# Kernel tuning notes

Hardware: AMD Instinct MI355X
Metric: run time of the kernel (lower is better)

## Reference

```python
import jax, jax.numpy as jnp
import numpy as np

B, T, F, H = 2048, 16, 768, 1024  # batch(nodes), timesteps, 3*input_size, hidden_size


def setup_inputs() -> dict:
    key = jax.random.key(0)
    k1, k2, k3 = jax.random.split(key, 3)
    s_ih = 1.0 / np.sqrt(F)
    s_hh = 1.0 / np.sqrt(H)
    return {
        "x": jax.random.normal(k1, (B, T, F), dtype=jnp.float32),
        "W_ih": jax.random.normal(k2, (F, 4 * H), dtype=jnp.float32) * s_ih,
        "W_hh": jax.random.normal(k3, (H, 4 * H), dtype=jnp.float32) * s_hh,
        "b": jnp.zeros((4 * H,), dtype=jnp.float32),
    }


def reference(x, W_ih, W_hh, b):
    # Batched equivalent of the original per-sample python loop:
    # each sample's [T, F] sequence runs through the LSTM; the final hidden
    # state [H] per sample is concatenated and reshaped to (-1, B).
    Bb, Tt, Ff = x.shape
    Hh = W_hh.shape[0]
    x_t = jnp.swapaxes(x, 0, 1)  # [T, B, F]

    def step(carry, xt):
        h, c = carry
        gates = xt @ W_ih + h @ W_hh + b  # [B, 4H]
        i, f, g, o = jnp.split(gates, 4, axis=-1)
        c = jax.nn.sigmoid(f) * c + jax.nn.sigmoid(i) * jnp.tanh(g)
        h = jax.nn.sigmoid(o) * jnp.tanh(c)
        return (h, c), None

    h0 = jnp.zeros((Bb, Hh), dtype=x.dtype)
    (h, _), _ = jax.lax.scan(step, (h0, h0), x_t)
    # torch.cat over batch of [H] vectors -> flat [B*H], then reshape(-1, B)
    return h.reshape(-1).reshape(-1, Bb)
```

## Files before the change

kernel.cpp:

```cpp
#include <hip/hip_runtime.h>
#include <hip/hip_bf16.h>
#include <stdint.h>

#define B_  2048
#define T_  16
#define F_  768
#define H_  1024
#define G4_ 4096

typedef __attribute__((ext_vector_type(8))) __bf16 bf16x8;
typedef __attribute__((ext_vector_type(4))) float  f32x4;

static __device__ __forceinline__ unsigned short f2bf(float f) {
    union { float f; uint32_t u; } v; v.f = f;
    uint32_t u = v.u;
    uint32_t r = (u + 0x7fffu + ((u >> 16) & 1u)) >> 16;
    return (unsigned short)r;
}
static __device__ __forceinline__ unsigned short f2h(float f) {
    union { _Float16 h; unsigned short u; } v; v.h = (_Float16)f; return v.u;
}
static __device__ __forceinline__ float h2f(unsigned short u) {
    union { _Float16 h; unsigned short u; } v; v.u = u; return (float)v.h;
}
static __device__ __forceinline__ float sigf(float x) {
    return 1.0f / (1.0f + __expf(-x));
}
static __device__ __forceinline__ float tanhfast(float x) {
    return 2.0f / (1.0f + __expf(-2.0f * x)) - 1.0f;
}

#define GLOAD_LDS16(gsrc, ldst)                                                       \
    __builtin_amdgcn_global_load_lds((const __attribute__((address_space(1))) void*)(gsrc), \
                                     (__attribute__((address_space(3))) void*)(ldst), \
                                     16, 0, 0)


__global__ void convert_x_kernel(const float* __restrict__ x,
                                 unsigned short* __restrict__ xbf, int n4) {
    int idx = blockIdx.x * blockDim.x + threadIdx.x;
    if (idx >= n4) return;
    float4 v = *(const float4*)(x + (size_t)idx * 4);
    ushort4 o;
    o.x = f2bf(v.x); o.y = f2bf(v.y); o.z = f2bf(v.z); o.w = f2bf(v.w);
    *(ushort4*)(xbf + (size_t)idx * 4) = o;
}

__global__ void transpose_w_kernel(const float* __restrict__ w,
                                   unsigned short* __restrict__ wt, int K, int mode) {
    __shared__ float tile[32][33];
    int nb = blockIdx.x * 32;
    int kb = blockIdx.y * 32;
    int tx = threadIdx.x, ty = threadIdx.y;
    #pragma unroll
    for (int i = 0; i < 32; i += 8)
        tile[ty + i][tx] = w[(size_t)(kb + ty + i) * G4_ + nb + tx];
    __syncthreads();
    #pragma unroll
    for (int i = 0; i < 32; i += 8) {
        int n = nb + ty + i;
        int g = n >> 10;
        int j = n & 1023;
        int np = mode ? ((j >> 4) * 64 + g * 16 + (j & 15))
                      : ((j >> 6) * 256 + g * 64 + ((j >> 4) & 3) * 16 + (j & 15));
        wt[(size_t)np * K + kb + tx] = f2bf(tile[tx][ty + i]);
    }
}


#define STAGE4(bufi, kind, half, gbase, ld, rowbase, kt) do {                         \
    const int kel_ = (kt) * 64;                                                       \
    _Pragma("unroll")                                                                 \
    for (int r2 = 0; r2 < 2; ++r2) {                                                  \
        const int rih_ = r2 * 64 + (tid >> 3);                                        \
        const int ch_  = (tid & 7) ^ (rih_ & 7);                                      \
        GLOAD_LDS16((gbase) + (size_t)((rowbase) + (half) * 128 + rih_) * (ld)        \
                            + kel_ + ch_ * 8,                                         \
                    &lds[bufi][kind][half][r2 * 4096 + tid * 8]);                     \
    }                                                                                 \
} while (0)

#define RD4_A(half_, mb)                                                              \
    _Pragma("unroll")                                                                 \
    for (int mm = 0; mm < 4; ++mm) {                                                  \
        const int row_ = ((mb) + mm) * 32 + wm * 16 + fr;                             \
        _Pragma("unroll")                                                             \
        for (int kk = 0; kk < 2; ++kk)                                                \
            Afr[mm][kk] = *(const bf16x8*)&lds[buf][0][half_]                         \
                [(row_ & 127) * 64 + (((kk * 4 + fq) ^ (row_ & 7)) * 8)];             \
    }

#define RD4_B(half_, nb)                                                              \
    _Pragma("unroll")                                                                 \
    for (int nn = 0; nn < 2; ++nn) {                                                  \
        const int row_ = ((nb) + nn) * 64 + wn * 16 + fr;                             \
        _Pragma("unroll")                                                             \
        for (int kk = 0; kk < 2; ++kk)                                                \
            Bfr[(nb) + nn][kk] = *(const bf16x8*)&lds[buf][1][half_]                  \
                [(row_ & 127) * 64 + (((kk * 4 + fq) ^ (row_ & 7)) * 8)];             \
    }

#define MFMAQ(mb, nb)                                                                 \
    __builtin_amdgcn_s_setprio(1);                                                    \
    _Pragma("unroll")                                                                 \
    for (int mm = 0; mm < 4; ++mm)                                                    \
        _Pragma("unroll")                                                             \
        for (int nn = 0; nn < 2; ++nn)                                                \
            _Pragma("unroll")                                                         \
            for (int kk = 0; kk < 2; ++kk)                                            \
                acc[(mb) + mm][(nb) + nn] = __builtin_amdgcn_mfma_f32_16x16x32_bf16(  \
                    Afr[mm][kk], Bfr[(nb) + nn][kk], acc[(mb) + mm][(nb) + nn], 0, 0, 0); \
    __builtin_amdgcn_s_setprio(0);

#define WAITV4  asm volatile("s_waitcnt vmcnt(10)" ::: "memory");                     \
                __builtin_amdgcn_sched_barrier(0);
#define BARR4   __builtin_amdgcn_s_barrier();                                         \
                __builtin_amdgcn_sched_barrier(0);

#define EPIX(pbn)                                                                     \
    {                                                                                 \
        const int j_ = (pbn) * 64 + wn * 16 + fr;                                     \
        _Pragma("unroll")                                                             \
        for (int mm = 0; mm < 8; ++mm) {                                              \
            _Pragma("unroll")                                                         \
            for (int rr = 0; rr < 4; ++rr) {                                          \
                int row_ = bm0 + mm * 32 + wm * 16 + fq * 4 + rr;                     \
                int tt_ = row_ & 15, bb_ = row_ >> 4;                                 \
                ushort4 o_;                                                           \
                o_.x = f2h(acc[mm][0][rr]);                                           \
                o_.y = f2h(acc[mm][1][rr]);                                           \
                o_.z = f2h(acc[mm][2][rr]);                                           \
                o_.w = f2h(acc[mm][3][rr]);                                           \
                *(ushort4*)(gx + (((size_t)tt_ * B_ + bb_) * H_ + j_) * 4) = o_;      \
            }                                                                         \
        }                                                                             \
    }

__global__ __launch_bounds__(512, 2) void xgemm8p_kernel(
        const unsigned short* __restrict__ xbf,
        const unsigned short* __restrict__ wih_t,
        unsigned short* __restrict__ gx) {
    __shared__ __align__(16) unsigned short lds[2][2][2][8192];

    const int bid = blockIdx.x;
    const int xcd = bid & 7;
    const int i   = bid >> 3;
    const int bnp = i & 7;
    const int bm  = xcd * 16 + (i >> 3);
    const int bm0 = bm * 256;
    const int bn00 = bnp * 512;

    const int tid = threadIdx.x;
    const int wid = tid >> 6, lane = tid & 63;
    const int wm = wid >> 2, wn = wid & 3;
    const int fr = lane & 15, fq = lane >> 4;

    f32x4 acc[8][4] = {};

    STAGE4(0, 0, 0, xbf, F_, bm0, 0);
    STAGE4(0, 1, 0, wih_t, F_, bn00, 0);
    STAGE4(0, 1, 1, wih_t, F_, bn00, 0);
    STAGE4(0, 0, 1, xbf, F_, bm0, 0);
    STAGE4(1, 0, 0, xbf, F_, bm0, 1);
    STAGE4(1, 1, 0, wih_t, F_, bn00, 1);
    STAGE4(1, 1, 1, wih_t, F_, bn00, 1);
    WAITV4; BARR4;

    for (int kt = 0; kt < 24; ++kt) {
        const int buf = kt & 1, nbuf = buf ^ 1;
        const int k1 = (kt + 1 < 24) ? kt + 1 : 23;
        const int k2 = (kt + 2 < 24) ? kt + 2 : 23;
        const int a1 = (k1 >= 12) ? k1 - 12 : k1;
        const int a2 = (k2 >= 12) ? k2 - 12 : k2;
        const int bb2 = bn00 + ((k2 >= 12) ? 256 : 0);
        bf16x8 Afr[4][2]; bf16x8 Bfr[4][2];
        RD4_A(0, 0); RD4_B(0, 0);
        STAGE4(nbuf, 0, 1, xbf, F_, bm0, a1);
        WAITV4; BARR4;
        MFMAQ(0, 0); BARR4;
        RD4_B(1, 2);
        STAGE4(buf, 0, 0, xbf, F_, bm0, a2);
        WAITV4; BARR4;
        MFMAQ(0, 2); BARR4;
        RD4_A(1, 4);
        STAGE4(buf, 1, 0, wih_t, F_, bb2, a2);
        BARR4;
        MFMAQ(4, 0); BARR4;
        STAGE4(buf, 1, 1, wih_t, F_, bb2, a2);
        WAITV4; BARR4;
        MFMAQ(4, 2); BARR4;
        if (kt == 11) {
            EPIX(bnp * 2);
            #pragma unroll
            for (int mm = 0; mm < 8; ++mm)
                #pragma unroll
                for (int nf = 0; nf < 4; ++nf)
                    #pragma unroll
                    for (int q = 0; q < 4; ++q) acc[mm][nf][q] = 0.0f;
        }
    }
    EPIX(bnp * 2 + 1);
}


#define STA6(slot, kt) do {                                                           \
    const int kel_ = (kt) * 64;                                                       \
    _Pragma("unroll")                                                                 \
    for (int r2 = 0; r2 < 2; ++r2) {                                                  \
        const int rih_ = r2 * 32 + (tid >> 3);                                        \
        const int ch_  = (tid & 7) ^ (rih_ & 7);                                      \
        GLOAD_LDS16(hprev + (size_t)(bm0 + rih_) * H_ + kel_ + ch_ * 8,               \
                    &ldsA[slot][r2 * 2048 + tid * 8]);                                \
    }                                                                                 \
} while (0)

#define STB6(slot, rowbase, kt) do {                                                  \
    const int kel_ = (kt) * 64;                                                       \
    _Pragma("unroll")                                                                 \
    for (int r4 = 0; r4 < 4; ++r4) {                                                  \
        const int rih_ = r4 * 32 + (tid >> 3);                                        \
        const int ch_  = (tid & 7) ^ (rih_ & 7);                                      \
        GLOAD_LDS16(whh_t + (size_t)((rowbase) + rih_) * H_ + kel_ + ch_ * 8,         \
                    &ldsB[slot][r4 * 2048 + tid * 8]);                                \
    }                                                                                 \
} while (0)

#define RD_A6(slot, AR)                                                               \
    _Pragma("unroll")                                                                 \
    for (int mm = 0; mm < 2; ++mm) {                                                  \
        const int row_ = wm * 32 + mm * 16 + fr;                                      \
        _Pragma("unroll")                                                             \
        for (int kk = 0; kk < 2; ++kk)                                                \
            AR[mm][kk] = *(const bf16x8*)&ldsA[slot]                                  \
                [row_ * 64 + (((kk * 4 + fq) ^ (row_ & 7)) * 8)];                     \
    }

#define RD_B6(slot, BF)                                                               \
    _Pragma("unroll")                                                                 \
    for (int nf = 0; nf < 4; ++nf) {                                                  \
        const int rowb_ = wn * 64 + nf * 16 + fr;                                     \
        _Pragma("unroll")                                                             \
        for (int kk = 0; kk < 2; ++kk)                                                \
            BF[nf][kk] = *(const bf16x8*)&ldsB[slot]                                  \
                [rowb_ * 64 + (((kk * 4 + fq) ^ (rowb_ & 7)) * 8)];                   \
    }

#define MFMA16S(AR, BF)                                                               \
    __builtin_amdgcn_s_setprio(1);                                                    \
    _Pragma("unroll")                                                                 \
    for (int mm = 0; mm < 2; ++mm)                                                    \
        _Pragma("unroll")                                                             \
        for (int nf = 0; nf < 4; ++nf)                                                \
            _Pragma("unroll")                                                         \
            for (int kk = 0; kk < 2; ++kk)                                            \
                acc[mm][nf] = __builtin_amdgcn_mfma_f32_16x16x32_bf16(                \
                    AR[mm][kk], BF[nf][kk], acc[mm][nf], 0, 0, 0);                    \
    __builtin_amdgcn_s_setprio(0);

#define LGKM0 asm volatile("s_waitcnt lgkmcnt(0)" ::: "memory");
#define BARR  __builtin_amdgcn_s_barrier();

__global__ __launch_bounds__(256, 2) void lstm_step_dp_kernel(
        const unsigned short* __restrict__ hprev,
        const unsigned short* __restrict__ whh_t,
        const unsigned short* __restrict__ gx,
        const float* __restrict__ bias,
        float* __restrict__ c,
        unsigned short* __restrict__ hnext,
        float* __restrict__ hout,
        int t, int last) {
    __shared__ __align__(16) unsigned short ldsA[3][4096];
    __shared__ __align__(16) unsigned short ldsB[3][8192];

    const int bid = blockIdx.x;
    const int xcd = bid & 7;
    const int i   = bid >> 3;
    const int pair = i & 1;
    const int bm  = i >> 1;
    const int bn_base = xcd * 4 + pair * 2;
    const int bm0 = bm * 64;

    const int tid = threadIdx.x;
    const int wid = tid >> 6, lane = tid & 63;
    const int wm = wid >> 1, wn = wid & 1;
    const int fr = lane & 15, fq = lane >> 4;

    const int j0 = (bn_base * 2 + wn) * 16 + fr;
    const int j1 = ((bn_base + 1) * 2 + wn) * 16 + fr;
    const float bi0 = bias[j0], bf0 = bias[H_ + j0], bg0 = bias[2 * H_ + j0], bo0 = bias[3 * H_ + j0];
    const float bi1 = bias[j1], bf1 = bias[H_ + j1], bg1 = bias[2 * H_ + j1], bo1 = bias[3 * H_ + j1];

    f32x4 acc[2][4] = {};
    ushort4 gpre[2][4];
    float   cpre[2][4];

    STA6(0, 0); STB6(0, bn_base * 128, 0);
    STA6(1, 1); STB6(1, bn_base * 128, 1);
    asm volatile("s_waitcnt vmcnt(6)" ::: "memory");
    BARR;

    for (int kt = 0; kt < 32; ++kt) {
        const int s_  = kt % 3;
        const int s2_ = (kt + 2) % 3;
        const int k2  = (kt + 2 < 32) ? kt + 2 : 31;
        const int ak2 = k2 & 15;
        const int brb2 = (bn_base + (k2 >> 4)) * 128;
        bf16x8 Am[2][2], Bf[4][2];
        RD_A6(s_, Am);
        RD_B6(s_, Bf);
        STA6(s2_, ak2);
        STB6(s2_, brb2, ak2);
        if (kt == 13 || kt == 29) {
            const int p_ = kt >> 4;
            const int jp_ = p_ ? j1 : j0;
            #pragma unroll
            for (int mm = 0; mm < 2; ++mm)
                #pragma unroll
                for (int rr = 0; rr < 4; ++rr) {
                    int row_ = bm0 + wm * 32 + mm * 16 + fq * 4 + rr;
                    gpre[mm][rr] = *(const ushort4*)(gx + (((size_t)t * B_ + row_) * H_ + jp_) * 4);
                    cpre[mm][rr] = c[(size_t)row_ * H_ + jp_];
                }
        }
        LGKM0;
        MFMA16S(Am, Bf);
        if (kt == 13 || kt == 14 || kt == 29 || kt == 30)
            asm volatile("s_waitcnt vmcnt(22)" ::: "memory");
        else
            asm volatile("s_waitcnt vmcnt(6)" ::: "memory");
        BARR;
        if (kt == 15) {
            #pragma unroll
            for (int mm = 0; mm < 2; ++mm) {
                #pragma unroll
                for (int rr = 0; rr < 4; ++rr) {
                    int row_ = bm0 + wm * 32 + mm * 16 + fq * 4 + rr;
                    ushort4 g4 = gpre[mm][rr];
                    float gi = acc[mm][0][rr] + bi0 + h2f(g4.x);
                    float gf = acc[mm][1][rr] + bf0 + h2f(g4.y);
                    float gg = acc[mm][2][rr] + bg0 + h2f(g4.z);
                    float go = acc[mm][3][rr] + bo0 + h2f(g4.w);
                    float cn = sigf(gf) * cpre[mm][rr] + sigf(gi) * tanhfast(gg);
                    float hv = sigf(go) * tanhfast(cn);
                    size_t off = (size_t)row_ * H_ + j0;
                    c[off] = cn;
                    hnext[off] = f2bf(hv);
                    if (last) hout[off] = hv;
                }
            }
            #pragma unroll
            for (int mm = 0; mm < 2; ++mm)
                #pragma unroll
                for (int nf = 0; nf < 4; ++nf)
                    #pragma unroll
                    for (int q = 0; q < 4; ++q) acc[mm][nf][q] = 0.0f;
        }
    }

    #pragma unroll
    for (int mm = 0; mm < 2; ++mm) {
        #pragma unroll
        for (int rr = 0; rr < 4; ++rr) {
            int row_ = bm0 + wm * 32 + mm * 16 + fq * 4 + rr;
            ushort4 g4 = gpre[mm][rr];
            float gi = acc[mm][0][rr] + bi1 + h2f(g4.x);
            float gf = acc[mm][1][rr] + bf1 + h2f(g4.y);
            float gg = acc[mm][2][rr] + bg1 + h2f(g4.z);
            float go = acc[mm][3][rr] + bo1 + h2f(g4.w);
            float cn = sigf(gf) * cpre[mm][rr] + sigf(gi) * tanhfast(gg);
            float hv = sigf(go) * tanhfast(cn);
            size_t off = (size_t)row_ * H_ + j1;
            c[off] = cn;
            hnext[off] = f2bf(hv);
            if (last) hout[off] = hv;
        }
    }
}


__global__ void cell0_kernel(const unsigned short* __restrict__ gx,
                             const float* __restrict__ bias,
                             float* __restrict__ c,
                             unsigned short* __restrict__ hbf) {
    int idx = blockIdx.x * blockDim.x + threadIdx.x;
    int b = idx >> 10;
    int j = idx & 1023;
    ushort4 g4 = *(const ushort4*)(gx + ((size_t)b * H_ + j) * 4);
    float gi = bias[j]          + h2f(g4.x);
    float gg = bias[2 * H_ + j] + h2f(g4.z);
    float go = bias[3 * H_ + j] + h2f(g4.w);
    float cn = sigf(gi) * tanhfast(gg);
    float hv = sigf(go) * tanhfast(cn);
    size_t off = (size_t)b * H_ + j;
    c[off] = cn;
    hbf[off] = f2bf(hv);
}


extern "C" void kernel_launch(void* const* d_in, const int* in_sizes, int n_in,
                              void* d_out, int out_size, void* d_ws, size_t ws_size,
                              hipStream_t stream) {
    const float* x    = (const float*)d_in[0];
    const float* Wih  = (const float*)d_in[1];
    const float* Whh  = (const float*)d_in[2];
    const float* bias = (const float*)d_in[3];
    float* out = (float*)d_out;

    char* ws = (char*)d_ws;
    unsigned short* xbf   = (unsigned short*)(ws);
    unsigned short* wih_t = (unsigned short*)(ws + 50331648);
    unsigned short* whh_t = (unsigned short*)(ws + 56623104);
    unsigned short* hbf0  = (unsigned short*)(ws + 65011712);
    unsigned short* hbf1  = (unsigned short*)(ws + 69206016);
    float*          c     = (float*)(ws + 73400320);
    unsigned short* gx    = (unsigned short*)(ws + 81788928);

    int n4 = B_ * T_ * F_ / 4;
    hipLaunchKernelGGL(convert_x_kernel, dim3((n4 + 255) / 256), dim3(256), 0, stream,
                       x, xbf, n4);
    hipLaunchKernelGGL(transpose_w_kernel, dim3(G4_ / 32, F_ / 32), dim3(32, 8), 0, stream,
                       Wih, wih_t, F_, 0);
    hipLaunchKernelGGL(transpose_w_kernel, dim3(G4_ / 32, H_ / 32), dim3(32, 8), 0, stream,
                       Whh, whh_t, H_, 1);

    hipLaunchKernelGGL(xgemm8p_kernel, dim3(1024), dim3(512), 0, stream,
                       xbf, wih_t, gx);

    hipLaunchKernelGGL(cell0_kernel, dim3(B_ * H_ / 256), dim3(256), 0, stream,
                       gx, bias, c, hbf0);

    for (int t = 1; t < T_; ++t) {
        unsigned short* hr = (t & 1) ? hbf0 : hbf1;
        unsigned short* hw = (t & 1) ? hbf1 : hbf0;
        hipLaunchKernelGGL(lstm_step_dp_kernel, dim3(512), dim3(256), 0, stream,
                           hr, whh_t, gx, bias, c, hw, out, t, (t == T_ - 1) ? 1 : 0);
    }
}
```

Measured before the change: 841.1 us.

## Fuse prep kernels into one launch and fold cell0 into the input GEMM

Merges the x conversion and the two weight transposes into a single block-indexed prep kernel. Restructures the input-projection GEMM so each block computes a single 256-column tile over 2048 blocks, replacing the earlier scheme of two tiles per block with a mid-loop epilogue. Fuses the t=0 LSTM cell update into the GEMM epilogue, so timestep-0 gates are never written to or re-read from global memory and the separate cell0 launch disappears. The cost removed is launch overhead and one gx round trip; the risk is a different tile schedule and occupancy for the GEMM.

Result: faster. 736.9 us (-12.4%).

```diff
diff --git a/kernel.cpp b/kernel.cpp
--- a/kernel.cpp
+++ b/kernel.cpp
@@ -36,22 +36,28 @@
                                      16, 0, 0)
 
 
-__global__ void convert_x_kernel(const float* __restrict__ x,
-                                 unsigned short* __restrict__ xbf, int n4) {
-    int idx = blockIdx.x * blockDim.x + threadIdx.x;
-    if (idx >= n4) return;
-    float4 v = *(const float4*)(x + (size_t)idx * 4);
-    ushort4 o;
-    o.x = f2bf(v.x); o.y = f2bf(v.y); o.z = f2bf(v.z); o.w = f2bf(v.w);
-    *(ushort4*)(xbf + (size_t)idx * 4) = o;
-}
-
-__global__ void transpose_w_kernel(const float* __restrict__ w,
-                                   unsigned short* __restrict__ wt, int K, int mode) {
+__global__ void prep_kernel(const float* __restrict__ x, unsigned short* __restrict__ xbf,
+                            const float* __restrict__ Wih, unsigned short* __restrict__ wih_t,
+                            const float* __restrict__ Whh, unsigned short* __restrict__ whh_t) {
+    const int bid = blockIdx.x;
+    const int tid = threadIdx.x;
+    if (bid < 24576) {
+        int idx = bid * 256 + tid;
+        float4 v = *(const float4*)(x + (size_t)idx * 4);
+        ushort4 o;
+        o.x = f2bf(v.x); o.y = f2bf(v.y); o.z = f2bf(v.z); o.w = f2bf(v.w);
+        *(ushort4*)(xbf + (size_t)idx * 4) = o;
+        return;
+    }
     __shared__ float tile[32][33];
-    int nb = blockIdx.x * 32;
-    int kb = blockIdx.y * 32;
-    int tx = threadIdx.x, ty = threadIdx.y;
+    const float* w;
+    unsigned short* wt;
+    int K, mode, idx;
+    if (bid < 24576 + 3072) { w = Wih; wt = wih_t; K = F_; mode = 0; idx = bid - 24576; }
+    else                    { w = Whh; wt = whh_t; K = H_; mode = 1; idx = bid - 27648; }
+    int nb = (idx & 127) * 32;
+    int kb = (idx >> 7) * 32;
+    int tx = tid & 31, ty = tid >> 5;
     #pragma unroll
     for (int i = 0; i < 32; i += 8)
         tile[ty + i][tx] = w[(size_t)(kb + ty + i) * G4_ + nb + tx];
@@ -117,38 +123,58 @@
 #define BARR4   __builtin_amdgcn_s_barrier();                                         \
                 __builtin_amdgcn_sched_barrier(0);
 
-#define EPIX(pbn)                                                                     \
-    {                                                                                 \
-        const int j_ = (pbn) * 64 + wn * 16 + fr;                                     \
-        _Pragma("unroll")                                                             \
-        for (int mm = 0; mm < 8; ++mm) {                                              \
-            _Pragma("unroll")                                                         \
-            for (int rr = 0; rr < 4; ++rr) {                                          \
-                int row_ = bm0 + mm * 32 + wm * 16 + fq * 4 + rr;                     \
-                int tt_ = row_ & 15, bb_ = row_ >> 4;                                 \
-                ushort4 o_;                                                           \
-                o_.x = f2h(acc[mm][0][rr]);                                           \
-                o_.y = f2h(acc[mm][1][rr]);                                           \
-                o_.z = f2h(acc[mm][2][rr]);                                           \
-                o_.w = f2h(acc[mm][3][rr]);                                           \
-                *(ushort4*)(gx + (((size_t)tt_ * B_ + bb_) * H_ + j_) * 4) = o_;      \
-            }                                                                         \
-        }                                                                             \
-    }
-
-__global__ __launch_bounds__(512, 2) void xgemm8p_kernel(
+#define KLOOP4(ABASE, ALD, BBASE, BLD, NT)                                            \
+    STAGE4(0, 0, 0, ABASE, ALD, bm0, 0);                                              \
+    STAGE4(0, 1, 0, BBASE, BLD, bn0, 0);                                              \
+    STAGE4(0, 1, 1, BBASE, BLD, bn0, 0);                                              \
+    STAGE4(0, 0, 1, ABASE, ALD, bm0, 0);                                              \
+    STAGE4(1, 0, 0, ABASE, ALD, bm0, 1);                                              \
+    STAGE4(1, 1, 0, BBASE, BLD, bn0, 1);                                              \
+    STAGE4(1, 1, 1, BBASE, BLD, bn0, 1);                                              \
+    WAITV4; BARR4;                                                                    \
+    for (int kt = 0; kt < (NT); ++kt) {                                               \
+        const int buf = kt & 1, nbuf = buf ^ 1;                                       \
+        const int k1 = (kt + 1 < (NT)) ? kt + 1 : (NT) - 1;                           \
+        const int k2 = (kt + 2 < (NT)) ? kt + 2 : (NT) - 1;                           \
+        bf16x8 Afr[4][2]; bf16x8 Bfr[4][2];                                           \
+                                                                             \
+        RD4_A(0, 0); RD4_B(0, 0);                                                     \
+        STAGE4(nbuf, 0, 1, ABASE, ALD, bm0, k1);                                      \
+        WAITV4; BARR4;                                                                \
+        MFMAQ(0, 0); BARR4;                                                           \
+                                                                             \
+        RD4_B(1, 2);                                                                  \
+        STAGE4(buf, 0, 0, ABASE, ALD, bm0, k2);                                       \
+        WAITV4; BARR4;                                                                \
+        MFMAQ(0, 2); BARR4;                                                           \
+                                                                             \
+        RD4_A(1, 4);                                                                  \
+        STAGE4(buf, 1, 0, BBASE, BLD, bn0, k2);                                       \
+        BARR4;                                                                        \
+        MFMAQ(4, 0); BARR4;                                                           \
+                                                                             \
+        STAGE4(buf, 1, 1, BBASE, BLD, bn0, k2);                                       \
+        WAITV4; BARR4;                                                                \
+        MFMAQ(4, 2); BARR4;                                                           \
+    }
+
+__global__ __launch_bounds__(512, 2) void xgemm8f_kernel(
         const unsigned short* __restrict__ xbf,
         const unsigned short* __restrict__ wih_t,
-        unsigned short* __restrict__ gx) {
+        unsigned short* __restrict__ gx,
+        const float* __restrict__ bias,
+        float* __restrict__ c,
+        unsigned short* __restrict__ hbf0) {
     __shared__ __align__(16) unsigned short lds[2][2][2][8192];
 
     const int bid = blockIdx.x;
     const int xcd = bid & 7;
     const int i   = bid >> 3;
-    const int bnp = i & 7;
-    const int bm  = xcd * 16 + (i >> 3);
-    const int bm0 = bm * 256;
-    const int bn00 = bnp * 512;
+    const int bmg = i >> 6;
+    const int r   = i & 63;
+    const int bn  = r >> 2;
+    const int bm  = xcd * 16 + bmg * 4 + (r & 3);
+    const int bm0 = bm * 256, bn0 = bn * 256;
 
     const int tid = threadIdx.x;
     const int wid = tid >> 6, lane = tid & 63;
@@ -157,49 +183,38 @@
 
     f32x4 acc[8][4] = {};
 
-    STAGE4(0, 0, 0, xbf, F_, bm0, 0);
-    STAGE4(0, 1, 0, wih_t, F_, bn00, 0);
-    STAGE4(0, 1, 1, wih_t, F_, bn00, 0);
-    STAGE4(0, 0, 1, xbf, F_, bm0, 0);
-    STAGE4(1, 0, 0, xbf, F_, bm0, 1);
-    STAGE4(1, 1, 0, wih_t, F_, bn00, 1);
-    STAGE4(1, 1, 1, wih_t, F_, bn00, 1);
-    WAITV4; BARR4;
-
-    for (int kt = 0; kt < 24; ++kt) {
-        const int buf = kt & 1, nbuf = buf ^ 1;
-        const int k1 = (kt + 1 < 24) ? kt + 1 : 23;
-        const int k2 = (kt + 2 < 24) ? kt + 2 : 23;
-        const int a1 = (k1 >= 12) ? k1 - 12 : k1;
-        const int a2 = (k2 >= 12) ? k2 - 12 : k2;
-        const int bb2 = bn00 + ((k2 >= 12) ? 256 : 0);
-        bf16x8 Afr[4][2]; bf16x8 Bfr[4][2];
-        RD4_A(0, 0); RD4_B(0, 0);
-        STAGE4(nbuf, 0, 1, xbf, F_, bm0, a1);
-        WAITV4; BARR4;
-        MFMAQ(0, 0); BARR4;
-        RD4_B(1, 2);
-        STAGE4(buf, 0, 0, xbf, F_, bm0, a2);
-        WAITV4; BARR4;
-        MFMAQ(0, 2); BARR4;
-        RD4_A(1, 4);
-        STAGE4(buf, 1, 0, wih_t, F_, bb2, a2);
-        BARR4;
-        MFMAQ(4, 0); BARR4;
-        STAGE4(buf, 1, 1, wih_t, F_, bb2, a2);
-        WAITV4; BARR4;
-        MFMAQ(4, 2); BARR4;
-        if (kt == 11) {
-            EPIX(bnp * 2);
-            #pragma unroll
-            for (int mm = 0; mm < 8; ++mm)
-                #pragma unroll
-                for (int nf = 0; nf < 4; ++nf)
-                    #pragma unroll
-                    for (int q = 0; q < 4; ++q) acc[mm][nf][q] = 0.0f;
+    KLOOP4(xbf, F_, wih_t, F_, 12)
+
+    const int j = bn * 64 + wn * 16 + fr;
+    float bi_ = 0.f, bg_ = 0.f, bo_ = 0.f;
+    if (fq == 0) {
+        bi_ = bias[j]; bg_ = bias[2 * H_ + j]; bo_ = bias[3 * H_ + j];
+    }
+    #pragma unroll
+    for (int mm = 0; mm < 8; ++mm) {
+        #pragma unroll
+        for (int rr = 0; rr < 4; ++rr) {
+            int row = bm0 + mm * 32 + wm * 16 + fq * 4 + rr;
+            int tt = row & 15, bb = row >> 4;
+            ushort4 o;
+            o.x = f2h(acc[mm][0][rr]);
+            o.y = f2h(acc[mm][1][rr]);
+            o.z = f2h(acc[mm][2][rr]);
+            o.w = f2h(acc[mm][3][rr]);
+            if (tt != 0) {
+                *(ushort4*)(gx + (((size_t)tt * B_ + bb) * H_ + j) * 4) = o;
+            } else {
+                float gi = bi_ + h2f(o.x);
+                float gg = bg_ + h2f(o.z);
+                float go = bo_ + h2f(o.w);
+                float cn = sigf(gi) * tanhfast(gg);
+                float hv = sigf(go) * tanhfast(cn);
+                size_t off = (size_t)bb * H_ + j;
+                c[off] = cn;
+                hbf0[off] = f2bf(hv);
+            }
         }
     }
-    EPIX(bnp * 2 + 1);
 }
 
 
@@ -378,25 +393,6 @@
 }
 
 
-__global__ void cell0_kernel(const unsigned short* __restrict__ gx,
-                             const float* __restrict__ bias,
-                             float* __restrict__ c,
-                             unsigned short* __restrict__ hbf) {
-    int idx = blockIdx.x * blockDim.x + threadIdx.x;
-    int b = idx >> 10;
-    int j = idx & 1023;
-    ushort4 g4 = *(const ushort4*)(gx + ((size_t)b * H_ + j) * 4);
-    float gi = bias[j]          + h2f(g4.x);
-    float gg = bias[2 * H_ + j] + h2f(g4.z);
-    float go = bias[3 * H_ + j] + h2f(g4.w);
-    float cn = sigf(gi) * tanhfast(gg);
-    float hv = sigf(go) * tanhfast(cn);
-    size_t off = (size_t)b * H_ + j;
-    c[off] = cn;
-    hbf[off] = f2bf(hv);
-}
-
-
 extern "C" void kernel_launch(void* const* d_in, const int* in_sizes, int n_in,
                               void* d_out, int out_size, void* d_ws, size_t ws_size,
                               hipStream_t stream) {
@@ -415,19 +411,11 @@
     float*          c     = (float*)(ws + 73400320);
     unsigned short* gx    = (unsigned short*)(ws + 81788928);
 
-    int n4 = B_ * T_ * F_ / 4;
-    hipLaunchKernelGGL(convert_x_kernel, dim3((n4 + 255) / 256), dim3(256), 0, stream,
-                       x, xbf, n4);
-    hipLaunchKernelGGL(transpose_w_kernel, dim3(G4_ / 32, F_ / 32), dim3(32, 8), 0, stream,
-                       Wih, wih_t, F_, 0);
-    hipLaunchKernelGGL(transpose_w_kernel, dim3(G4_ / 32, H_ / 32), dim3(32, 8), 0, stream,
-                       Whh, whh_t, H_, 1);
-
-    hipLaunchKernelGGL(xgemm8p_kernel, dim3(1024), dim3(512), 0, stream,
-                       xbf, wih_t, gx);
-
-    hipLaunchKernelGGL(cell0_kernel, dim3(B_ * H_ / 256), dim3(256), 0, stream,
-                       gx, bias, c, hbf0);
+    hipLaunchKernelGGL(prep_kernel, dim3(24576 + 3072 + 4096), dim3(256), 0, stream,
+                       x, xbf, Wih, wih_t, Whh, whh_t);
+
+    hipLaunchKernelGGL(xgemm8f_kernel, dim3(2048), dim3(512), 0, stream,
+                       xbf, wih_t, gx, bias, c, hbf0);
 
     for (int t = 1; t < T_; ++t) {
         unsigned short* hr = (t & 1) ? hbf0 : hbf1;
```

## Merge prep kernels, fuse timestep-0 cell into input GEMM, retile over M

Applied to the files above, without the earlier changes.

Combines the x conversion and both weight transposes into a single prep launch. The input-projection GEMM is retiled so each block holds one 256-column slice of W_ih and walks four 256-row M tiles, reusing the B operand across them. The timestep-0 LSTM cell is computed inside the GEMM epilogue, which removes the separate cell0 kernel and the gx write and read for t=0. The cost is half as many GEMM blocks (512) with longer loops and a divergent epilogue branch.

Result: faster. 724.9 us (-13.8%).

```diff
diff --git a/kernel.cpp b/kernel.cpp
--- a/kernel.cpp
+++ b/kernel.cpp
@@ -36,22 +36,28 @@
                                      16, 0, 0)
 
 
-__global__ void convert_x_kernel(const float* __restrict__ x,
-                                 unsigned short* __restrict__ xbf, int n4) {
-    int idx = blockIdx.x * blockDim.x + threadIdx.x;
-    if (idx >= n4) return;
-    float4 v = *(const float4*)(x + (size_t)idx * 4);
-    ushort4 o;
-    o.x = f2bf(v.x); o.y = f2bf(v.y); o.z = f2bf(v.z); o.w = f2bf(v.w);
-    *(ushort4*)(xbf + (size_t)idx * 4) = o;
-}
-
-__global__ void transpose_w_kernel(const float* __restrict__ w,
-                                   unsigned short* __restrict__ wt, int K, int mode) {
+__global__ void prep_kernel(const float* __restrict__ x, unsigned short* __restrict__ xbf,
+                            const float* __restrict__ Wih, unsigned short* __restrict__ wih_t,
+                            const float* __restrict__ Whh, unsigned short* __restrict__ whh_t) {
+    const int bid = blockIdx.x;
+    const int tid = threadIdx.x;
+    if (bid < 24576) {
+        int idx = bid * 256 + tid;
+        float4 v = *(const float4*)(x + (size_t)idx * 4);
+        ushort4 o;
+        o.x = f2bf(v.x); o.y = f2bf(v.y); o.z = f2bf(v.z); o.w = f2bf(v.w);
+        *(ushort4*)(xbf + (size_t)idx * 4) = o;
+        return;
+    }
     __shared__ float tile[32][33];
-    int nb = blockIdx.x * 32;
-    int kb = blockIdx.y * 32;
-    int tx = threadIdx.x, ty = threadIdx.y;
+    const float* w;
+    unsigned short* wt;
+    int K, mode, idx;
+    if (bid < 24576 + 3072) { w = Wih; wt = wih_t; K = F_; mode = 0; idx = bid - 24576; }
+    else                    { w = Whh; wt = whh_t; K = H_; mode = 1; idx = bid - 27648; }
+    int nb = (idx & 127) * 32;
+    int kb = (idx >> 7) * 32;
+    int tx = tid & 31, ty = tid >> 5;
     #pragma unroll
     for (int i = 0; i < 32; i += 8)
         tile[ty + i][tx] = w[(size_t)(kb + ty + i) * G4_ + nb + tx];
@@ -117,80 +123,99 @@
 #define BARR4   __builtin_amdgcn_s_barrier();                                         \
                 __builtin_amdgcn_sched_barrier(0);
 
-#define EPIX(pbn)                                                                     \
+#define EPIX_M(mbase)                                                                 \
     {                                                                                 \
-        const int j_ = (pbn) * 64 + wn * 16 + fr;                                     \
         _Pragma("unroll")                                                             \
         for (int mm = 0; mm < 8; ++mm) {                                              \
             _Pragma("unroll")                                                         \
             for (int rr = 0; rr < 4; ++rr) {                                          \
-                int row_ = bm0 + mm * 32 + wm * 16 + fq * 4 + rr;                     \
+                int row_ = (mbase) + mm * 32 + wm * 16 + fq * 4 + rr;                 \
                 int tt_ = row_ & 15, bb_ = row_ >> 4;                                 \
                 ushort4 o_;                                                           \
                 o_.x = f2h(acc[mm][0][rr]);                                           \
                 o_.y = f2h(acc[mm][1][rr]);                                           \
                 o_.z = f2h(acc[mm][2][rr]);                                           \
                 o_.w = f2h(acc[mm][3][rr]);                                           \
-                *(ushort4*)(gx + (((size_t)tt_ * B_ + bb_) * H_ + j_) * 4) = o_;      \
+                if (tt_ != 0) {                                                       \
+                    *(ushort4*)(gx + (((size_t)tt_ * B_ + bb_) * H_ + j) * 4) = o_;   \
+                } else {                                                              \
+                    float gi_ = bi_ + h2f(o_.x);                                      \
+                    float gg_ = bg_ + h2f(o_.z);                                      \
+                    float go_ = bo_ + h2f(o_.w);                                      \
+                    float cn_ = sigf(gi_) * tanhfast(gg_);                            \
+                    float hv_ = sigf(go_) * tanhfast(cn_);                            \
+                    size_t off_ = (size_t)bb_ * H_ + j;                               \
+                    c[off_] = cn_;                                                    \
+                    hbf0[off_] = f2bf(hv_);                                           \
+                }                                                                     \
             }                                                                         \
         }                                                                             \
     }
 
-__global__ __launch_bounds__(512, 2) void xgemm8p_kernel(
+__global__ __launch_bounds__(512, 2) void xgemm8m_kernel(
         const unsigned short* __restrict__ xbf,
         const unsigned short* __restrict__ wih_t,
-        unsigned short* __restrict__ gx) {
+        unsigned short* __restrict__ gx,
+        const float* __restrict__ bias,
+        float* __restrict__ c,
+        unsigned short* __restrict__ hbf0) {
     __shared__ __align__(16) unsigned short lds[2][2][2][8192];
 
     const int bid = blockIdx.x;
     const int xcd = bid & 7;
     const int i   = bid >> 3;
-    const int bnp = i & 7;
-    const int bm  = xcd * 16 + (i >> 3);
-    const int bm0 = bm * 256;
-    const int bn00 = bnp * 512;
+    const int bn  = xcd * 2 + (i & 1);
+    const int mg  = i >> 1;
+    const int bmb = mg * 1024;
+    const int bn0 = bn * 256;
 
     const int tid = threadIdx.x;
     const int wid = tid >> 6, lane = tid & 63;
     const int wm = wid >> 2, wn = wid & 3;
     const int fr = lane & 15, fq = lane >> 4;
 
+    const int j = bn * 64 + wn * 16 + fr;
+    float bi_ = 0.f, bg_ = 0.f, bo_ = 0.f;
+    if (fq == 0) {
+        bi_ = bias[j]; bg_ = bias[2 * H_ + j]; bo_ = bias[3 * H_ + j];
+    }
+
     f32x4 acc[8][4] = {};
 
-    STAGE4(0, 0, 0, xbf, F_, bm0, 0);
-    STAGE4(0, 1, 0, wih_t, F_, bn00, 0);
-    STAGE4(0, 1, 1, wih_t, F_, bn00, 0);
-    STAGE4(0, 0, 1, xbf, F_, bm0, 0);
-    STAGE4(1, 0, 0, xbf, F_, bm0, 1);
-    STAGE4(1, 1, 0, wih_t, F_, bn00, 1);
-    STAGE4(1, 1, 1, wih_t, F_, bn00, 1);
+    STAGE4(0, 0, 0, xbf, F_, bmb, 0);
+    STAGE4(0, 1, 0, wih_t, F_, bn0, 0);
+    STAGE4(0, 1, 1, wih_t, F_, bn0, 0);
+    STAGE4(0, 0, 1, xbf, F_, bmb, 0);
+    STAGE4(1, 0, 0, xbf, F_, bmb, 1);
+    STAGE4(1, 1, 0, wih_t, F_, bn0, 1);
+    STAGE4(1, 1, 1, wih_t, F_, bn0, 1);
     WAITV4; BARR4;
 
-    for (int kt = 0; kt < 24; ++kt) {
+    for (int kt = 0; kt < 48; ++kt) {
         const int buf = kt & 1, nbuf = buf ^ 1;
-        const int k1 = (kt + 1 < 24) ? kt + 1 : 23;
-        const int k2 = (kt + 2 < 24) ? kt + 2 : 23;
-        const int a1 = (k1 >= 12) ? k1 - 12 : k1;
-        const int a2 = (k2 >= 12) ? k2 - 12 : k2;
-        const int bb2 = bn00 + ((k2 >= 12) ? 256 : 0);
+        const int k1 = (kt + 1 < 48) ? kt + 1 : 47;
+        const int k2 = (kt + 2 < 48) ? kt + 2 : 47;
+        const int a1b = bmb + (k1 / 12) * 256, a1k = k1 % 12;
+        const int a2b = bmb + (k2 / 12) * 256, a2k = k2 % 12;
+        const int b2k = k2 % 12;
         bf16x8 Afr[4][2]; bf16x8 Bfr[4][2];
         RD4_A(0, 0); RD4_B(0, 0);
-        STAGE4(nbuf, 0, 1, xbf, F_, bm0, a1);
+        STAGE4(nbuf, 0, 1, xbf, F_, a1b, a1k);
         WAITV4; BARR4;
         MFMAQ(0, 0); BARR4;
         RD4_B(1, 2);
-        STAGE4(buf, 0, 0, xbf, F_, bm0, a2);
+        STAGE4(buf, 0, 0, xbf, F_, a2b, a2k);
         WAITV4; BARR4;
         MFMAQ(0, 2); BARR4;
         RD4_A(1, 4);
-        STAGE4(buf, 1, 0, wih_t, F_, bb2, a2);
+        STAGE4(buf, 1, 0, wih_t, F_, bn0, b2k);
         BARR4;
         MFMAQ(4, 0); BARR4;
-        STAGE4(buf, 1, 1, wih_t, F_, bb2, a2);
+        STAGE4(buf, 1, 1, wih_t, F_, bn0, b2k);
         WAITV4; BARR4;
         MFMAQ(4, 2); BARR4;
-        if (kt == 11) {
-            EPIX(bnp * 2);
+        if ((kt % 12) == 11) {
+            EPIX_M(bmb + (kt / 12) * 256);
             #pragma unroll
             for (int mm = 0; mm < 8; ++mm)
                 #pragma unroll
@@ -199,7 +224,6 @@
                     for (int q = 0; q < 4; ++q) acc[mm][nf][q] = 0.0f;
         }
     }
-    EPIX(bnp * 2 + 1);
 }
 
 
@@ -378,25 +402,6 @@
 }
 
 
-__global__ void cell0_kernel(const unsigned short* __restrict__ gx,
-                             const float* __restrict__ bias,
-                             float* __restrict__ c,
-                             unsigned short* __restrict__ hbf) {
-    int idx = blockIdx.x * blockDim.x + threadIdx.x;
-    int b = idx >> 10;
-    int j = idx & 1023;
-    ushort4 g4 = *(const ushort4*)(gx + ((size_t)b * H_ + j) * 4);
-    float gi = bias[j]          + h2f(g4.x);
-    float gg = bias[2 * H_ + j] + h2f(g4.z);
-    float go = bias[3 * H_ + j] + h2f(g4.w);
-    float cn = sigf(gi) * tanhfast(gg);
-    float hv = sigf(go) * tanhfast(cn);
-    size_t off = (size_t)b * H_ + j;
-    c[off] = cn;
-    hbf[off] = f2bf(hv);
-}
-
-
 extern "C" void kernel_launch(void* const* d_in, const int* in_sizes, int n_in,
                               void* d_out, int out_size, void* d_ws, size_t ws_size,
                               hipStream_t stream) {
@@ -415,19 +420,11 @@
     float*          c     = (float*)(ws + 73400320);
     unsigned short* gx    = (unsigned short*)(ws + 81788928);
 
-    int n4 = B_ * T_ * F_ / 4;
-    hipLaunchKernelGGL(convert_x_kernel, dim3((n4 + 255) / 256), dim3(256), 0, stream,
-                       x, xbf, n4);
-    hipLaunchKernelGGL(transpose_w_kernel, dim3(G4_ / 32, F_ / 32), dim3(32, 8), 0, stream,
-                       Wih, wih_t, F_, 0);
-    hipLaunchKernelGGL(transpose_w_kernel, dim3(G4_ / 32, H_ / 32), dim3(32, 8), 0, stream,
-                       Whh, whh_t, H_, 1);
-
-    hipLaunchKernelGGL(xgemm8p_kernel, dim3(1024), dim3(512), 0, stream,
-                       xbf, wih_t, gx);
-
-    hipLaunchKernelGGL(cell0_kernel, dim3(B_ * H_ / 256), dim3(256), 0, stream,
-                       gx, bias, c, hbf0);
+    hipLaunchKernelGGL(prep_kernel, dim3(24576 + 3072 + 4096), dim3(256), 0, stream,
+                       x, xbf, Wih, wih_t, Whh, whh_t);
+
+    hipLaunchKernelGGL(xgemm8m_kernel, dim3(512), dim3(512), 0, stream,
+                       xbf, wih_t, gx, bias, c, hbf0);
 
     for (int t = 1; t < T_; ++t) {
         unsigned short* hr = (t & 1) ? hbf0 : hbf1;
```
